# Optimization experiments

Hardware: AMD Instinct MI355X
Metric: run time of the kernel (lower is better)

The kernel has to match this reference:

```python
import jax, jax.numpy as jnp
import numpy as np

COST_CLASS, COST_BBOX, COST_GIOU = 1.0, 5.0, 2.0


def _box_area(b):
    return (b[..., 2] - b[..., 0]) * (b[..., 3] - b[..., 1])


def _generalized_box_iou(b1, b2):
    # b1: (B,Q,4), b2: (B,N,4), xyxy -> (B,Q,N)
    a1 = _box_area(b1)[:, :, None]
    a2 = _box_area(b2)[:, None, :]
    lt = jnp.maximum(b1[:, :, None, :2], b2[:, None, :, :2])
    rb = jnp.minimum(b1[:, :, None, 2:], b2[:, None, :, 2:])
    wh = jnp.clip(rb - lt, 0.0)
    inter = wh[..., 0] * wh[..., 1]
    union = a1 + a2 - inter
    iou = inter / union
    lt_c = jnp.minimum(b1[:, :, None, :2], b2[:, None, :, :2])
    rb_c = jnp.maximum(b1[:, :, None, 2:], b2[:, None, :, 2:])
    wh_c = jnp.clip(rb_c - lt_c, 0.0)
    area_c = wh_c[..., 0] * wh_c[..., 1]
    return iou - (area_c - union) / area_c


@jax.jit
def _cost_matrix(pred_logits, pred_boxes, tgt_labels, tgt_boxes):
    B, Q, _ = pred_logits.shape
    N = tgt_labels.shape[1]
    out_prob = jax.nn.softmax(pred_logits, axis=-1)  # (B,Q,C+1)
    idx = jnp.broadcast_to(tgt_labels[:, None, :], (B, Q, N))
    cost_class = -jnp.take_along_axis(out_prob, idx, axis=-1)          # (B,Q,N)
    cost_bbox = jnp.abs(pred_boxes[:, :, None, :] - tgt_boxes[:, None, :, :]).sum(-1)  # L1 cdist
    cost_giou = -_generalized_box_iou(pred_boxes, tgt_boxes)
    return COST_CLASS * cost_class + COST_BBOX * cost_bbox + COST_GIOU * cost_giou


def _lsa(cost):
    """Shortest-augmenting-path Hungarian (Jonker-Volgenant style).
    cost: (n, m) with n <= m. Returns col4row[i] = assigned column of row i.
    Matches scipy.optimize.linear_sum_assignment (minimization)."""
    n, m = cost.shape
    INF = np.inf
    u = np.zeros(n + 1)
    v = np.zeros(m + 1)
    p = np.zeros(m + 1, dtype=np.int64)   # p[j] = row (1-indexed) assigned to col j
    way = np.zeros(m + 1, dtype=np.int64)
    for i in range(1, n + 1):
        p[0] = i
        j0 = 0
        minv = np.full(m + 1, INF)
        used = np.zeros(m + 1, dtype=bool)
        while True:
            used[j0] = True
            i0 = p[j0]
            cur = cost[i0 - 1] - u[i0] - v[1:]
            free = ~used[1:]
            upd = free & (cur < minv[1:])
            minv[1:][upd] = cur[upd]
            way[1:][upd] = j0
            cand = np.where(free, minv[1:], INF)
            j1 = int(np.argmin(cand)) + 1
            delta = cand[j1 - 1]
            uj = np.nonzero(used)[0]
            u[p[uj]] += delta
            v[uj] -= delta
            minv[~used] -= delta
            j0 = j1
            if p[j0] == 0:
                break
        while j0 != 0:
            j1 = way[j0]
            p[j0] = p[j1]
            j0 = j1
    col4row = np.zeros(n, dtype=np.int64)
    for j in range(1, m + 1):
        if p[j] != 0:
            col4row[p[j] - 1] = j - 1
    return col4row


def setup_inputs() -> dict:
    key = jax.random.key(0)
    k1, k2, k3, k4, k5 = jax.random.split(key, 5)
    B, Q, N, C1 = 64, 600, 80, 92

    def make_boxes(kx, ky, shape):
        xy = jax.random.uniform(kx, shape + (2,)) * 0.6
        wh = jax.random.uniform(ky, shape + (2,)) * 0.35 + 0.02
        return jnp.concatenate([xy, xy + wh], axis=-1)  # valid xyxy

    pred_logits = jax.random.normal(k1, (B, Q, C1), dtype=jnp.float32)
    pred_boxes = make_boxes(k2, k3, (B, Q))
    tgt_labels = jax.random.randint(k4, (B, N), 0, 91)
    tgt_boxes = make_boxes(k5, jax.random.fold_in(k5, 1), (B, N))
    return {"pred_logits": pred_logits, "pred_boxes": pred_boxes,
            "tgt_labels": tgt_labels, "tgt_boxes": tgt_boxes}


def reference(pred_logits, pred_boxes, tgt_labels, tgt_boxes):
    # Batched cost-matrix build on device, then host Hungarian per sample
    # (mirrors the original's .cpu().numpy() + scipy linear_sum_assignment).
    C = np.asarray(_cost_matrix(pred_logits, pred_boxes, tgt_labels, tgt_boxes))  # (B,Q,N)
    B, Q, N = C.shape
    rows = np.empty((B, N), dtype=np.int64)
    cols = np.empty((B, N), dtype=np.int64)
    for b in range(B):
        q_of_t = _lsa(C[b].T)              # transpose: N <= Q; query index per target
        order = np.argsort(q_of_t, kind="stable")
        rows[b] = q_of_t[order]            # sorted query (row) indices
        cols[b] = order                    # matching target (col) indices
    return jnp.asarray(rows), jnp.asarray(cols)
```

## Files before the change

kernel.cpp:

```cpp
#include <hip/hip_runtime.h>
#include <math.h>

#define BB 64
#define QQ 600
#define NT 80
#define NC 92
#define SLOTS 10
#define NTILE 10
#define NTHR 256
#define NWAVE 4
#define MAXROUNDS 48
#define SPINCAP (1 << 20)
#define MAGIC 0x5A17C0DE

__global__ __launch_bounds__(256) void matcher_kernel(
    const float* __restrict__ logits,
    const float* __restrict__ pboxes,
    const int*   __restrict__ tlabels,
    const float* __restrict__ tboxes,
    float* __restrict__ cost,
    float* __restrict__ pm1,
    float* __restrict__ pm2,
    int*   __restrict__ pmj,
    int*   __restrict__ done,
    int* __restrict__ rows_out,
    int* __restrict__ cols_out)
{
    __shared__ float tile[64 * 93];
    __shared__ float s_m[64], s_s[64];
    __shared__ float s_pm[4 * 64], s_ps[4 * 64];
    __shared__ float s_tb[NT * 4];
    __shared__ int   s_tl[NT];
    __shared__ double vA[QQ];
    __shared__ double u[NT];
    __shared__ double bidm1[NT], bidm2[NT];
    __shared__ int    bidj[NT], bidver[NT];
    __shared__ int    pA[QQ];
    __shared__ int    verA[QQ];
    __shared__ int    colrow[QQ];
    __shared__ int    assigned[NT];
    __shared__ int    plist[NT];
    __shared__ int    pcnt;
    __shared__ int    wayA[QQ];
    __shared__ int    c4r[NT];
    __shared__ int    djkA[NT];

    const int g   = blockIdx.x;
    const int b   = g / NTILE;
    const int tix = g % NTILE;
    const int tid = threadIdx.x;
    const int qq  = tid & 63;
    const int wv  = tid >> 6;
    const float* C = cost + (size_t)b * NT * QQ;

    {
        const int q0 = tix * 64;
        const int nq = min(64, QQ - q0);
        const float* src = logits + ((size_t)b * QQ + q0) * NC;
        for (int idx = tid; idx < nq * NC; idx += 256) {
            const int r = idx / NC;
            tile[r * 93 + (idx - r * NC)] = src[idx];
        }
        for (int i = tid; i < NT * 4; i += 256) s_tb[i] = tboxes[b * NT * 4 + i];
        for (int i = tid; i < NT;     i += 256) s_tl[i] = tlabels[b * NT + i];
        __syncthreads();

        if (tid < nq) {
            const float* r = &tile[tid * 93];
            float m0 = r[0], m1 = r[1], m2 = r[2], m3 = r[3];
            for (int c = 4; c < NC; c += 4) {
                m0 = fmaxf(m0, r[c]);   m1 = fmaxf(m1, r[c+1]);
                m2 = fmaxf(m2, r[c+2]); m3 = fmaxf(m3, r[c+3]);
            }
            const float m = fmaxf(fmaxf(m0, m1), fmaxf(m2, m3));
            float s0 = 0.f, s1 = 0.f, s2 = 0.f, s3 = 0.f;
            for (int c = 0; c < NC; c += 4) {
                s0 += expf(r[c]   - m); s1 += expf(r[c+1] - m);
                s2 += expf(r[c+2] - m); s3 += expf(r[c+3] - m);
            }
            s_m[tid] = m; s_s[tid] = (s0 + s1) + (s2 + s3);
        }
        __syncthreads();

        const bool valid = qq < nq;
        float px1 = 0.f, py1 = 0.f, px2 = 0.f, py2 = 0.f, pa = 0.f, m = 0.f, s = 1.f;
        if (valid) {
            const float* pb = pboxes + ((size_t)b * QQ + q0 + qq) * 4;
            px1 = pb[0]; py1 = pb[1]; px2 = pb[2]; py2 = pb[3];
            pa  = (px2 - px1) * (py2 - py1);
            m = s_m[qq]; s = s_s[qq];
        }
        float* crow = cost + (size_t)b * NT * QQ + q0 + qq;
        const int q = q0 + qq;

        for (int tt = 0; tt < 20; ++tt) {
            const int t = wv * 20 + tt;
            float costv = INFINITY;
            if (valid) {
                const int lbl = s_tl[t];
                const float cc = -(expf(tile[qq * 93 + lbl] - m) / s);
                const float tx1 = s_tb[t*4+0], ty1 = s_tb[t*4+1];
                const float tx2 = s_tb[t*4+2], ty2 = s_tb[t*4+3];
                const float cb = fabsf(px1-tx1) + fabsf(py1-ty1)
                               + fabsf(px2-tx2) + fabsf(py2-ty2);
                const float ta = (tx2 - tx1) * (ty2 - ty1);
                const float iw = fmaxf(fminf(px2, tx2) - fmaxf(px1, tx1), 0.f);
                const float ih = fmaxf(fminf(py2, ty2) - fmaxf(py1, ty1), 0.f);
                const float inter = iw * ih;
                const float uni   = pa + ta - inter;
                const float iou   = inter / uni;
                const float cw = fmaxf(fmaxf(px2, tx2) - fminf(px1, tx1), 0.f);
                const float ch = fmaxf(fmaxf(py2, ty2) - fminf(py1, ty1), 0.f);
                const float ac = cw * ch;
                const float giou = iou - (ac - uni) / ac;
                costv = (1.0f * cc + 5.0f * cb) + 2.0f * (-giou);
                crow[(size_t)t * QQ] = costv;
            }
            float b1 = costv, b2 = INFINITY; int bj = valid ? q : QQ;
            #pragma unroll
            for (int off = 32; off > 0; off >>= 1) {
                const float o1 = __shfl_xor(b1, off);
                const float o2 = __shfl_xor(b2, off);
                const int   oj = __shfl_xor(bj, off);
                if (o1 < b1 || (o1 == b1 && oj < bj)) {
                    b2 = fminf(b1, o2); b1 = o1; bj = oj;
                } else {
                    b2 = fminf(o1, b2);
                }
            }
            if (qq == 0) {
                const size_t idx = ((size_t)b * NT + t) * NTILE + tix;
                pm1[idx] = b1; pm2[idx] = b2; pmj[idx] = bj;
            }
        }
    }
    __syncthreads();
    if (tid == 0)
        __hip_atomic_store(&done[b * 16 + tix], MAGIC, __ATOMIC_RELEASE, __HIP_MEMORY_SCOPE_AGENT);
    if (tix != 0) return;

    if (tid < NTILE) {
        int spins = 0;
        while (__hip_atomic_load(&done[b * 16 + tid], __ATOMIC_ACQUIRE, __HIP_MEMORY_SCOPE_AGENT) != MAGIC) {
            __builtin_amdgcn_s_sleep(8);
            if (++spins > SPINCAP) break;
        }
    }
    __syncthreads();

    for (int c = tid; c < QQ; c += NTHR) { pA[c] = -1; verA[c] = 0; vA[c] = 0.0; }
    if (tid < NT) { assigned[tid] = 0; bidver[tid] = 0; }
    __syncthreads();

    if (tid < NT) {
        const int t = tid;
        const float* p1 = pm1 + ((size_t)b * NT + t) * NTILE;
        const float* p2 = pm2 + ((size_t)b * NT + t) * NTILE;
        const int*   pj = pmj + ((size_t)b * NT + t) * NTILE;
        float m1 = INFINITY, m2 = INFINITY; int j1 = QQ;
        for (int k = 0; k < NTILE; ++k) {
            const float a1 = p1[k], a2 = p2[k];
            const int   aj = pj[k];
            if (a1 < m1) { m2 = fminf(m1, a2); m1 = a1; j1 = aj; }
            else         { m2 = fminf(m2, a1); }
        }
        bidm1[t] = (double)m1; bidm2[t] = (double)m2; bidj[t] = j1;
        u[t] = (double)m1;
    }
    __syncthreads();

    for (int round = 0; round < MAXROUNDS; ++round) {
        for (int c = tid; c < QQ; c += NTHR) colrow[c] = 0x7fffffff;
        if (tid == 0) pcnt = 0;
        __syncthreads();
        if (tid < NT && !assigned[tid]) {
            const int j = bidj[tid];
            if (bidver[tid] == verA[j]) atomicMin(&colrow[j], tid);
        }
        __syncthreads();
        if (tid < NT && !assigned[tid]) {
            const int i = tid, j = bidj[i];
            if (bidver[i] == verA[j] && colrow[j] == i) {
                const double m1 = bidm1[i], m2 = bidm2[i];
                const int prev = pA[j];
                pA[j] = i;
                verA[j] = verA[j] + 1;
                vA[j] -= (m2 - m1);
                u[i] = m2;
                assigned[i] = 1;
                if (prev >= 0) assigned[prev] = 0;
            }
        }
        __syncthreads();
        if (tid < NT && !assigned[tid]) { const int k = atomicAdd(&pcnt, 1); plist[k] = tid; }
        __syncthreads();
        const int np = pcnt;
        if (np == 0) break;
        for (int idx = wv; idx < np; idx += NWAVE) {
            const int i = plist[idx];
            const float* rp = C + (size_t)i * QQ;
            float rowv[SLOTS];
            #pragma unroll
            for (int k = 0; k < SLOTS; ++k) { const int c = qq + 64*k; rowv[k] = (c < QQ) ? rp[c] : 0.f; }
            double m1 = INFINITY, m2 = INFINITY; int j1 = QQ;
            #pragma unroll
            for (int k = 0; k < SLOTS; ++k) {
                const int c = qq + 64 * k;
                if (c < QQ) {
                    const double key = (double)rowv[k] - vA[c];
                    if (key < m1)      { m2 = m1; m1 = key; j1 = c; }
                    else if (key < m2) { m2 = key; }
                }
            }
            #pragma unroll
            for (int off = 32; off > 0; off >>= 1) {
                const double om1 = __shfl_xor(m1, off);
                const int    oj1 = __shfl_xor(j1, off);
                const double om2 = __shfl_xor(m2, off);
                if (om1 < m1 || (om1 == m1 && oj1 < j1)) {
                    m2 = fmin(m1, om2); m1 = om1; j1 = oj1;
                } else {
                    m2 = fmin(om1, m2);
                }
            }
            if (qq == 0) {
                bidm1[i] = m1; bidm2[i] = m2; bidj[i] = j1;
                bidver[i] = verA[j1];
                u[i] = m1;
            }
        }
        __syncthreads();
    }

    if (wv != 0) return;
    const int lane = qq;

    int nd = 0;
    for (int i = 0; i < NT; ++i) {
        if (!assigned[i]) { if (lane == 0) djkA[nd] = i; ++nd; }
    }

    double v_[SLOTS], minv_[SLOTS];
    int p_[SLOTS];
    #pragma unroll
    for (int k = 0; k < SLOTS; ++k) {
        const int c = lane + 64 * k;
        v_[k] = (c < QQ) ? vA[c] : 0.0;
        p_[k] = (c < QQ) ? pA[c] : -1;
    }

    float rowv[SLOTS];
    for (int ii = 0; ii < nd; ++ii) {
        const int i = djkA[ii];
        #pragma unroll
        for (int k = 0; k < SLOTS; ++k) minv_[k] = INFINITY;
        unsigned usedm = 0;
        int j0 = -1;
        double ui0 = u[i];
        {
            const float* rp = C + (size_t)i * QQ;
            #pragma unroll
            for (int k = 0; k < SLOTS; ++k) { const int c = lane + 64*k; rowv[k] = (c < QQ) ? rp[c] : 0.f; }
        }
        int j1, i1;

        for (;;) {
            if (j0 >= 0 && (j0 & 63) == lane) usedm |= 1u << (j0 >> 6);

            double bestv = INFINITY; int bestc = QQ;
            #pragma unroll
            for (int k = 0; k < SLOTS; ++k) {
                const int c = lane + 64 * k;
                if (c < QQ && !((usedm >> k) & 1u)) {
                    const double cur = ((double)rowv[k] - ui0) - v_[k];
                    if (cur < minv_[k]) { minv_[k] = cur; wayA[c] = j0; }
                    if (minv_[k] < bestv) { bestv = minv_[k]; bestc = c; }
                }
            }
            #pragma unroll
            for (int off = 32; off > 0; off >>= 1) {
                const double ov = __shfl_xor(bestv, off);
                const int    oc = __shfl_xor(bestc, off);
                if (ov < bestv || (ov == bestv && oc < bestc)) { bestv = ov; bestc = oc; }
            }
            const double delta = bestv;
            j1 = bestc;

            {
                const int slot = j1 >> 6, lj = j1 & 63;
                int myp = p_[0];
                #pragma unroll
                for (int k = 1; k < SLOTS; ++k) if (slot == k) myp = p_[k];
                i1 = __shfl(myp, lj);
            }

            double ui_next = 0.0;
            float rown[SLOTS];
            if (i1 >= 0) {
                ui_next = u[i1];
                const float* rp = C + (size_t)i1 * QQ;
                #pragma unroll
                for (int k = 0; k < SLOTS; ++k) { const int c = lane + 64*k; rown[k] = (c < QQ) ? rp[c] : 0.f; }
            }

            #pragma unroll
            for (int k = 0; k < SLOTS; ++k) {
                const int c = lane + 64 * k;
                if (c < QQ) {
                    if ((usedm >> k) & 1u) { v_[k] -= delta; u[p_[k]] += delta; }
                    else                     minv_[k] -= delta;
                }
            }
            if (lane == 0) u[i] += delta;

            j0 = j1;
            if (i1 < 0) break;
            ui0 = ui_next;
            #pragma unroll
            for (int k = 0; k < SLOTS; ++k) rowv[k] = rown[k];
        }

        if (lane == 0) {
            int jj = j1;
            while (jj >= 0) {
                const int pr = wayA[jj];
                pA[jj] = (pr < 0) ? i : pA[pr];
                jj = pr;
            }
        }
        #pragma unroll
        for (int k = 0; k < SLOTS; ++k) {
            const int c = lane + 64 * k;
            p_[k] = (c < QQ) ? pA[c] : -1;
        }
    }

    #pragma unroll
    for (int k = 0; k < SLOTS; ++k) {
        const int c = lane + 64 * k;
        if (c < QQ) { const int t = pA[c]; if (t >= 0) c4r[t] = c; }
    }
    for (int t = lane; t < NT; t += 64) {
        const int c = c4r[t];
        int rank = 0;
        for (int t2 = 0; t2 < NT; ++t2) rank += (c4r[t2] < c) ? 1 : 0;
        rows_out[b * NT + rank] = c;
        cols_out[b * NT + rank] = t;
    }
}

extern "C" void kernel_launch(void* const* d_in, const int* in_sizes, int n_in,
                              void* d_out, int out_size, void* d_ws, size_t ws_size,
                              hipStream_t stream) {
    (void)in_sizes; (void)n_in; (void)out_size; (void)ws_size;
    const float* logits  = (const float*)d_in[0];
    const float* pboxes  = (const float*)d_in[1];
    const int*   tlabels = (const int*)d_in[2];
    const float* tboxes  = (const float*)d_in[3];
    float* cost = (float*)d_ws;
    float* pm1  = cost + (size_t)BB * NT * QQ;
    float* pm2  = pm1  + (size_t)BB * NT * NTILE;
    int*   pmj  = (int*)(pm2 + (size_t)BB * NT * NTILE);
    int*   done = pmj + (size_t)BB * NT * NTILE;
    int*   out  = (int*)d_out;

    matcher_kernel<<<dim3(BB * NTILE), NTHR, 0, stream>>>(
        logits, pboxes, tlabels, tboxes, cost, pm1, pm2, pmj, done,
        out, out + BB * NT);
}
```

Baseline: 129.1 us.

## Replace parallel auction rounds with single-wave sequential Gale-Shapley augmentation queue

Drops the multi-round block-wide auction phase, which needed four block barriers per round. Only the initial conflict resolution stays parallel. The remaining unassigned rows are then processed by one wavefront through a FIFO queue, where each bid evicts the previous owner and requeues it. Ties and queue overflow fall back to the existing Dijkstra augmentation. This removes barrier cost and the version bookkeeping, but serialises the bidding onto a single wave, which can lengthen the critical path when many evictions occur.

```diff
diff --git a/kernel.cpp b/kernel.cpp
--- a/kernel.cpp
+++ b/kernel.cpp
@@ -9,7 +9,7 @@
 #define NTILE 10
 #define NTHR 256
 #define NWAVE 4
-#define MAXROUNDS 48
+#define GSCAP 320
 #define SPINCAP (1 << 20)
 #define MAGIC 0x5A17C0DE
 
@@ -28,19 +28,18 @@
 {
     __shared__ float tile[64 * 93];
     __shared__ float s_m[64], s_s[64];
-    __shared__ float s_pm[4 * 64], s_ps[4 * 64];
     __shared__ float s_tb[NT * 4];
     __shared__ int   s_tl[NT];
     __shared__ double vA[QQ];
     __shared__ double u[NT];
     __shared__ double bidm1[NT], bidm2[NT];
-    __shared__ int    bidj[NT], bidver[NT];
+    __shared__ int    bidj[NT];
     __shared__ int    pA[QQ];
-    __shared__ int    verA[QQ];
     __shared__ int    colrow[QQ];
     __shared__ int    assigned[NT];
     __shared__ int    plist[NT];
     __shared__ int    pcnt;
+    __shared__ int    gsq[GSCAP];
     __shared__ int    wayA[QQ];
     __shared__ int    c4r[NT];
     __shared__ int    djkA[NT];
@@ -148,8 +147,9 @@
     }
     __syncthreads();
 
-    for (int c = tid; c < QQ; c += NTHR) { pA[c] = -1; verA[c] = 0; vA[c] = 0.0; }
-    if (tid < NT) { assigned[tid] = 0; bidver[tid] = 0; }
+    for (int c = tid; c < QQ; c += NTHR) { pA[c] = -1; vA[c] = 0.0; colrow[c] = 0x7fffffff; }
+    if (tid < NT) assigned[tid] = 0;
+    if (tid == 0) pcnt = 0;
     __syncthreads();
 
     if (tid < NT) {
@@ -169,43 +169,42 @@
     }
     __syncthreads();
 
-    for (int round = 0; round < MAXROUNDS; ++round) {
-        for (int c = tid; c < QQ; c += NTHR) colrow[c] = 0x7fffffff;
-        if (tid == 0) pcnt = 0;
-        __syncthreads();
-        if (tid < NT && !assigned[tid]) {
-            const int j = bidj[tid];
-            if (bidver[tid] == verA[j]) atomicMin(&colrow[j], tid);
-        }
-        __syncthreads();
-        if (tid < NT && !assigned[tid]) {
-            const int i = tid, j = bidj[i];
-            if (bidver[i] == verA[j] && colrow[j] == i) {
-                const double m1 = bidm1[i], m2 = bidm2[i];
-                const int prev = pA[j];
-                pA[j] = i;
-                verA[j] = verA[j] + 1;
-                vA[j] -= (m2 - m1);
-                u[i] = m2;
-                assigned[i] = 1;
-                if (prev >= 0) assigned[prev] = 0;
-            }
-        }
-        __syncthreads();
-        if (tid < NT && !assigned[tid]) { const int k = atomicAdd(&pcnt, 1); plist[k] = tid; }
-        __syncthreads();
-        const int np = pcnt;
-        if (np == 0) break;
-        for (int idx = wv; idx < np; idx += NWAVE) {
-            const int i = plist[idx];
+    if (tid < NT) atomicMin(&colrow[bidj[tid]], tid);
+    __syncthreads();
+    if (tid < NT) {
+        const int i = tid, j = bidj[i];
+        if (colrow[j] == i) {
+            const double m1 = bidm1[i], m2 = bidm2[i];
+            pA[j] = i;
+            vA[j] -= (m2 - m1);
+            u[i] = m2;
+            assigned[i] = 1;
+        }
+    }
+    __syncthreads();
+    if (tid < NT && !assigned[tid]) { const int k = atomicAdd(&pcnt, 1); plist[k] = tid; }
+    __syncthreads();
+    const int np0 = pcnt;
+
+    if (wv != 0) return;
+    const int lane = qq;
+
+    int nd = 0;
+
+    {
+        int head = 0, tail = 0, steps = 0;
+        for (int k = 0; k < np0; ++k) gsq[tail++] = plist[k];
+        while (head < tail) {
+            const int i = gsq[head++];
+            if (++steps > GSCAP - NT) { djkA[nd++] = i; continue; }
             const float* rp = C + (size_t)i * QQ;
             float rowv[SLOTS];
             #pragma unroll
-            for (int k = 0; k < SLOTS; ++k) { const int c = qq + 64*k; rowv[k] = (c < QQ) ? rp[c] : 0.f; }
+            for (int k = 0; k < SLOTS; ++k) { const int c = lane + 64*k; rowv[k] = (c < QQ) ? rp[c] : 0.f; }
             double m1 = INFINITY, m2 = INFINITY; int j1 = QQ;
             #pragma unroll
             for (int k = 0; k < SLOTS; ++k) {
-                const int c = qq + 64 * k;
+                const int c = lane + 64 * k;
                 if (c < QQ) {
                     const double key = (double)rowv[k] - vA[c];
                     if (key < m1)      { m2 = m1; m1 = key; j1 = c; }
@@ -223,21 +222,22 @@
                     m2 = fmin(om1, m2);
                 }
             }
-            if (qq == 0) {
-                bidm1[i] = m1; bidm2[i] = m2; bidj[i] = j1;
-                bidver[i] = verA[j1];
-                u[i] = m1;
-            }
-        }
-        __syncthreads();
-    }
-
-    if (wv != 0) return;
-    const int lane = qq;
-
-    int nd = 0;
-    for (int i = 0; i < NT; ++i) {
-        if (!assigned[i]) { if (lane == 0) djkA[nd] = i; ++nd; }
+            if (lane == 0) u[i] = m1;
+            const int prev = pA[j1];
+            if (m1 < m2) {
+                if (lane == 0) {
+                    vA[j1] -= (m2 - m1);
+                    pA[j1] = i; u[i] = m2;
+                }
+                if (prev >= 0) {
+                    if (tail < GSCAP) gsq[tail++] = prev; else djkA[nd++] = prev;
+                }
+            } else if (prev < 0) {
+                if (lane == 0) { pA[j1] = i; u[i] = m2; }
+            } else {
+                djkA[nd++] = i;
+            }
+        }
     }
 
     double v_[SLOTS], minv_[SLOTS];
@@ -338,7 +338,7 @@
     #pragma unroll
     for (int k = 0; k < SLOTS; ++k) {
         const int c = lane + 64 * k;
-        if (c < QQ) { const int t = pA[c]; if (t >= 0) c4r[t] = c; }
+        if (c < QQ) { const int t = p_[k]; if (t >= 0) c4r[t] = c; }
     }
     for (int t = lane; t < NT; t += 64) {
         const int c = c4r[t];
```

Result: slower. 150.6 us (+16.6%).
